# Optimization experiments

Hardware: AMD Instinct MI355X
Metric: run time of the kernel (lower is better)

The kernel has to match this reference:

```python
import jax, jax.numpy as jnp
import numpy as np
from jax import lax

N_DEV = 10

def _branch(inp, w, b, g, bt, m, v):
    # Conv2d(3->4,k3,s1,p1) + BatchNorm2d(eval stats) + ReLU + MaxPool2d(2)
    y = lax.conv_general_dilated(inp, w, (1, 1), ((1, 1), (1, 1)),
                                 dimension_numbers=('NCHW', 'OIHW', 'NCHW'))
    y = y + b[None, :, None, None]
    scale = (g / jnp.sqrt(v + 1e-5))[None, :, None, None]
    y = (y - m[None, :, None, None]) * scale + bt[None, :, None, None]
    y = jnp.maximum(y, 0.0)
    y = lax.reduce_window(y, -jnp.inf, lax.max, (1, 1, 2, 2), (1, 1, 2, 2), 'VALID')
    return y.reshape(y.shape[0], -1)

def _forward(x, conv_w, conv_b, bn_gamma, bn_beta, bn_mean, bn_var,
             cut_w_big, cut_w_small, fc1_w, fc1_b, fc2_w, fc2_b,
             out_w, out_b, b_mat, h_mat, a_mat, indicator, noise):
    zs = []
    for n in range(N_DEV):
        if n <= 1:
            inp = x[:, :, 32 * n:32 * n + 32, :32]
        else:
            r = (16 * (n - 2)) % 64
            c = 32 + 16 * ((n - 2) // 4)
            inp = x[:, :, r:r + 16, c:c + 16]
        flat = _branch(inp, conv_w[n], conv_b[n], bn_gamma[n], bn_beta[n],
                       bn_mean[n], bn_var[n])
        w = cut_w_big[n] if n <= 1 else cut_w_small[n - 2]
        zs.append(flat @ w.T)  # [B, 256]
    z = jnp.stack(zs)                           # [n_dev, B, 256]
    transmit = z * b_mat[:, None, :]            # per-device precoding
    # indicator is one-hot over subcarriers: h_sel[n, j] = h_mat[n, k(j)]
    h_sel = jnp.einsum('jk,nkc->njc', indicator, h_mat)   # [n_dev, 256, 5]
    # h_vec[n, j] = sum(a_mat[j].T @ h_sel[n, j])
    h_vec = jnp.einsum('njc,jcm->nj', h_sel, a_mat)       # [n_dev, 256]
    received = jnp.sum(transmit * h_vec[:, None, :], axis=0)  # [B, 256]
    noise_term = jnp.einsum('jc,jcm->j', noise, a_mat)        # [256]
    received = received + noise_term[None, :]
    h1 = jnp.maximum(received, 0.0)
    h2 = jnp.maximum(h1 @ fc1_w.T + fc1_b, 0.0)
    h3 = jnp.maximum(h2 @ fc2_w.T + fc2_b, 0.0)
    logits = h3 @ out_w.T + out_b
    return jax.nn.log_softmax(logits, axis=1)

def setup_inputs() -> dict:
    key = jax.random.key(0)
    ks = jax.random.split(key, 12)
    B, K, s = 4096, 64, 0.02
    return {
        'x': jax.random.normal(ks[0], (B, 3, 64, 64), jnp.float32),
        'conv_w': jax.random.normal(ks[1], (10, 4, 3, 3, 3), jnp.float32) * s,
        'conv_b': jnp.zeros((10, 4), jnp.float32),
        'bn_gamma': jnp.ones((10, 4), jnp.float32),
        'bn_beta': jnp.zeros((10, 4), jnp.float32),
        'bn_mean': jnp.zeros((10, 4), jnp.float32),
        'bn_var': jnp.ones((10, 4), jnp.float32),
        'cut_w_big': jax.random.normal(ks[2], (2, 256, 1024), jnp.float32) * s,
        'cut_w_small': jax.random.normal(ks[3], (8, 256, 256), jnp.float32) * s,
        'fc1_w': jax.random.normal(ks[4], (128, 256), jnp.float32) * s,
        'fc1_b': jnp.zeros((128,), jnp.float32),
        'fc2_w': jax.random.normal(ks[5], (64, 128), jnp.float32) * s,
        'fc2_b': jnp.zeros((64,), jnp.float32),
        'out_w': jax.random.normal(ks[6], (10, 64), jnp.float32) * s,
        'out_b': jnp.zeros((10,), jnp.float32),
        'b_mat': jax.random.normal(ks[7], (10, 256), jnp.float32) * 0.1,
        'h_mat': jax.random.normal(ks[8], (10, K, 5), jnp.float32),
        'a_mat': jax.random.normal(ks[9], (256, 5, 5), jnp.float32) * 0.1,
        'indicator': jax.nn.one_hot(
            jax.random.randint(ks[10], (256,), 0, K), K, dtype=jnp.float32),
        'noise': jax.random.normal(ks[11], (256, 5), jnp.float32) * 0.1,
    }

def reference(x, conv_w, conv_b, bn_gamma, bn_beta, bn_mean, bn_var,
              cut_w_big, cut_w_small, fc1_w, fc1_b, fc2_w, fc2_b,
              out_w, out_b, b_mat, h_mat, a_mat, indicator, noise):
    return _forward(x, conv_w, conv_b, bn_gamma, bn_beta, bn_mean, bn_var,
                    cut_w_big, cut_w_small, fc1_w, fc1_b, fc2_w, fc2_b,
                    out_w, out_b, b_mat, h_mat, a_mat, indicator, noise)
```

## Files before the change

### kernel.cpp

```cpp
#include <hip/hip_runtime.h>
#include <math.h>

typedef __attribute__((ext_vector_type(8))) short bf16x8;
typedef __attribute__((ext_vector_type(4))) float f32x4;

static __device__ __forceinline__ short f2bf(float f) {
    union { float f; unsigned u; } v; v.f = f;
    unsigned r = v.u + 0x7FFFu + ((v.u >> 16) & 1u);
    return (short)(r >> 16);
}

__global__ __launch_bounds__(256) void k_build_w(
    const float* __restrict__ cut_w_big,
    const float* __restrict__ cut_w_small,
    const float* __restrict__ b_mat,
    const float* __restrict__ h_mat,
    const float* __restrict__ a_mat,
    const float* __restrict__ indicator,
    short* __restrict__ W)
{
    int bx = blockIdx.x;
    int tid0 = bx << 8;
    int j = tid0 >> 12;
    int kbase = tid0 & 4095;
    int n = (kbase < 2048) ? (kbase >> 10) : 2 + ((kbase - 2048) >> 8);

    float arow[5];
#pragma unroll
    for (int c = 0; c < 5; ++c) {
        float s = 0.f;
#pragma unroll
        for (int m = 0; m < 5; ++m) s += a_mat[j * 25 + c * 5 + m];
        arow[c] = s;
    }
    int lane = threadIdx.x & 63;
    float hs = 0.f;
#pragma unroll
    for (int c = 0; c < 5; ++c) hs += h_mat[(n * 64 + lane) * 5 + c] * arow[c];
    float v = indicator[j * 64 + lane] * hs;
#pragma unroll
    for (int off = 32; off >= 1; off >>= 1) v += __shfl_xor(v, off);
    float coeff = b_mat[n * 256 + j] * v;

    int tid = tid0 + threadIdx.x;
    int k = tid & 4095;
    float w;
    if (k < 2048) {
        w = cut_w_big[(((k >> 10) * 256 + j) << 10) + (k & 1023)];
    } else {
        int kk = k - 2048;
        w = cut_w_small[(((kk >> 8) * 256 + j) << 8) + (kk & 255)];
    }
    W[tid] = f2bf(w * coeff);
}

__global__ __launch_bounds__(256) void k_branch(
    const float* __restrict__ x,
    const float* __restrict__ conv_w,
    const float* __restrict__ conv_b,
    const float* __restrict__ bn_g,
    const float* __restrict__ bn_b,
    const float* __restrict__ bn_m,
    const float* __restrict__ bn_v,
    short* __restrict__ F)
{
    __shared__ float in_s[4320];
    __shared__ float bn_a[4], bn_c[4];
    int t = threadIdx.x;
    int bx = blockIdx.x;

    for (int i = t; i < 4320; i += 256) in_s[i] = 0.f;
    __syncthreads();

    if (bx < 8192) {
        int n = bx >> 12;
        int b = bx & 4095;
        int r0 = 32 * n;
        for (int i = t; i < 3072; i += 256) {
            int ci = i >> 10;
            int rem = i & 1023;
            int yy = rem >> 5;
            int xx = rem & 31;
            in_s[ci * 1224 + (yy + 1) * 36 + (xx + 1)] =
                x[((size_t)(b * 3 + ci) * 64 + r0 + yy) * 64 + xx];
        }
        if (t < 4) {
            float scale = bn_g[n * 4 + t] * rsqrtf(bn_v[n * 4 + t] + 1e-5f);
            bn_a[t] = scale;
            bn_c[t] = (conv_b[n * 4 + t] - bn_m[n * 4 + t]) * scale + bn_b[n * 4 + t];
        }
        __syncthreads();

        int py = t >> 4, px = t & 15;
        float win[3][4][4];
#pragma unroll
        for (int ci = 0; ci < 3; ++ci)
#pragma unroll
            for (int dy = 0; dy < 4; ++dy)
#pragma unroll
                for (int dx = 0; dx < 4; ++dx)
                    win[ci][dy][dx] = in_s[ci * 1224 + (2 * py + dy) * 36 + (2 * px + dx)];
        const float* wp = conv_w + n * 108;
#pragma unroll
        for (int co = 0; co < 4; ++co) {
            float s00 = 0.f, s01 = 0.f, s10 = 0.f, s11 = 0.f;
#pragma unroll
            for (int ci = 0; ci < 3; ++ci)
#pragma unroll
                for (int ky = 0; ky < 3; ++ky)
#pragma unroll
                    for (int kx = 0; kx < 3; ++kx) {
                        float wv = wp[co * 27 + ci * 9 + ky * 3 + kx];
                        s00 += win[ci][ky][kx] * wv;
                        s01 += win[ci][ky][kx + 1] * wv;
                        s10 += win[ci][ky + 1][kx] * wv;
                        s11 += win[ci][ky + 1][kx + 1] * wv;
                    }
            float a = bn_a[co], c2 = bn_c[co];
            float v0 = fmaxf(s00 * a + c2, 0.f);
            float v1 = fmaxf(s01 * a + c2, 0.f);
            float v2 = fmaxf(s10 * a + c2, 0.f);
            float v3 = fmaxf(s11 * a + c2, 0.f);
            F[(size_t)b * 4096 + n * 1024 + co * 256 + t] =
                f2bf(fmaxf(fmaxf(v0, v1), fmaxf(v2, v3)));
        }
    } else {
        int i2 = bx - 8192;
        int n = 2 + (i2 >> 10);
        int g = i2 & 1023;
        int b0 = g * 4;
        int r0 = 16 * ((n - 2) & 3);
        int c0 = 32 + 16 * ((n - 2) >> 2);
        for (int i = t; i < 3072; i += 256) {
            int ci = i >> 10;
            int rem = i & 1023;
            int img = rem >> 8;
            int yy = (rem >> 4) & 15;
            int xx = rem & 15;
            in_s[((ci * 4 + img) * 18 + yy + 1) * 20 + xx + 1] =
                x[((size_t)((b0 + img) * 3 + ci) * 64 + r0 + yy) * 64 + c0 + xx];
        }
        if (t < 4) {
            float scale = bn_g[n * 4 + t] * rsqrtf(bn_v[n * 4 + t] + 1e-5f);
            bn_a[t] = scale;
            bn_c[t] = (conv_b[n * 4 + t] - bn_m[n * 4 + t]) * scale + bn_b[n * 4 + t];
        }
        __syncthreads();

        int img = t >> 6;
        int pos = t & 63;
        int py = pos >> 3, px = pos & 7;
        float win[3][4][4];
#pragma unroll
        for (int ci = 0; ci < 3; ++ci)
#pragma unroll
            for (int dy = 0; dy < 4; ++dy)
#pragma unroll
                for (int dx = 0; dx < 4; ++dx)
                    win[ci][dy][dx] =
                        in_s[((ci * 4 + img) * 18 + 2 * py + dy) * 20 + (2 * px + dx)];
        const float* wp = conv_w + n * 108;
#pragma unroll
        for (int co = 0; co < 4; ++co) {
            float s00 = 0.f, s01 = 0.f, s10 = 0.f, s11 = 0.f;
#pragma unroll
            for (int ci = 0; ci < 3; ++ci)
#pragma unroll
                for (int ky = 0; ky < 3; ++ky)
#pragma unroll
                    for (int kx = 0; kx < 3; ++kx) {
                        float wv = wp[co * 27 + ci * 9 + ky * 3 + kx];
                        s00 += win[ci][ky][kx] * wv;
                        s01 += win[ci][ky][kx + 1] * wv;
                        s10 += win[ci][ky + 1][kx] * wv;
                        s11 += win[ci][ky + 1][kx + 1] * wv;
                    }
            float a = bn_a[co], c2 = bn_c[co];
            float v0 = fmaxf(s00 * a + c2, 0.f);
            float v1 = fmaxf(s01 * a + c2, 0.f);
            float v2 = fmaxf(s10 * a + c2, 0.f);
            float v3 = fmaxf(s11 * a + c2, 0.f);
            F[(size_t)(b0 + img) * 4096 + 2048 + (n - 2) * 256 + co * 64 + pos] =
                f2bf(fmaxf(fmaxf(v0, v1), fmaxf(v2, v3)));
        }
    }
}

__global__ __launch_bounds__(256) void k_gemm(
    const short* __restrict__ F,
    const short* __restrict__ W,
    float* __restrict__ P)
{
    __shared__ short As[128 * 64];
    __shared__ short Bs[128 * 64];
    int bx = blockIdx.x;
    int mt = bx & 31;
    int jt = (bx >> 5) & 1;
    int ks = bx >> 6;
    int t = threadIdx.x;
    int m0 = mt << 7, j0 = jt << 7;

    int lane = t & 63;
    int wave = t >> 6;
    int wm = wave & 1, wn = wave >> 1;
    int l16 = lane & 15, quad = lane >> 4;

    f32x4 acc[4][4];
#pragma unroll
    for (int i = 0; i < 4; ++i)
#pragma unroll
        for (int j = 0; j < 4; ++j) acc[i][j] = (f32x4){0.f, 0.f, 0.f, 0.f};

    for (int it = 0; it < 8; ++it) {
        int k0 = (ks << 9) + (it << 6);
#pragma unroll
        for (int r = 0; r < 4; ++r) {
            int c = (r << 8) + t;
            int row = c >> 3, s = c & 7;
            int g = s ^ (row & 7);
            const short* gpA = F + ((size_t)(m0 + row) << 12) + k0 + (g << 3);
            const short* gpB = W + ((size_t)(j0 + row) << 12) + k0 + (g << 3);
            __builtin_amdgcn_global_load_lds(
                (const __attribute__((address_space(1))) void*)gpA,
                (__attribute__((address_space(3))) void*)(As + (c << 3)), 16, 0, 0);
            __builtin_amdgcn_global_load_lds(
                (const __attribute__((address_space(1))) void*)gpB,
                (__attribute__((address_space(3))) void*)(Bs + (c << 3)), 16, 0, 0);
        }
        __syncthreads();
#pragma unroll
        for (int ks2 = 0; ks2 < 2; ++ks2) {
            bf16x8 af[4], bfr[4];
#pragma unroll
            for (int mi = 0; mi < 4; ++mi) {
                int row = (wm << 6) + (mi << 4) + l16;
                int q = (ks2 << 2) + quad;
                int sl = q ^ (row & 7);
                af[mi] = *(const bf16x8*)&As[(row << 6) + (sl << 3)];
            }
#pragma unroll
            for (int ni = 0; ni < 4; ++ni) {
                int row = (wn << 6) + (ni << 4) + l16;
                int q = (ks2 << 2) + quad;
                int sl = q ^ (row & 7);
                bfr[ni] = *(const bf16x8*)&Bs[(row << 6) + (sl << 3)];
            }
#pragma unroll
            for (int mi = 0; mi < 4; ++mi)
#pragma unroll
                for (int ni = 0; ni < 4; ++ni)
                    acc[mi][ni] = __builtin_amdgcn_mfma_f32_16x16x32_bf16(
                        af[mi], bfr[ni], acc[mi][ni], 0, 0, 0);
        }
        __syncthreads();
    }

    float* Pp = P + ((size_t)ks << 20);
#pragma unroll
    for (int mi = 0; mi < 4; ++mi)
#pragma unroll
        for (int ni = 0; ni < 4; ++ni) {
            int col = j0 + (wn << 6) + (ni << 4) + l16;
#pragma unroll
            for (int r = 0; r < 4; ++r) {
                int row = m0 + (wm << 6) + (mi << 4) + (quad << 2) + r;
                Pp[(size_t)row * 256 + col] = acc[mi][ni][r];
            }
        }
}

__global__ __launch_bounds__(256) void k_reduce(
    const float* __restrict__ P,
    const float* __restrict__ a_mat,
    const float* __restrict__ noise,
    float* __restrict__ R)
{
    int b = blockIdx.x;
    int j = threadIdx.x;
    float nt = 0.f;
#pragma unroll
    for (int c = 0; c < 5; ++c) {
        float ar = 0.f;
#pragma unroll
        for (int m = 0; m < 5; ++m) ar += a_mat[j * 25 + c * 5 + m];
        nt += noise[j * 5 + c] * ar;
    }
    float s = nt;
    size_t base = (size_t)b * 256 + j;
#pragma unroll
    for (int ks = 0; ks < 8; ++ks) s += P[((size_t)ks << 20) + base];
    R[base] = fmaxf(s, 0.f);
}

__global__ __launch_bounds__(256) void k_mlp(
    const float* __restrict__ R,
    const float* __restrict__ fc1_w, const float* __restrict__ fc1_b,
    const float* __restrict__ fc2_w, const float* __restrict__ fc2_b,
    const float* __restrict__ out_w, const float* __restrict__ out_b,
    float* __restrict__ out)
{
    __shared__ __align__(16) float Rt[8][260];
    __shared__ __align__(16) float H2[8][132];
    __shared__ __align__(16) float H3[8][68];
    __shared__ float LG[8][12];
    __shared__ float mrow[8], srow[8];
    int t = threadIdx.x;
    int b0 = blockIdx.x * 8;

    for (int i = t; i < 512; i += 256) {
        int r = i >> 6;
        int c4 = i & 63;
        *(float4*)&Rt[r][c4 * 4] = *(const float4*)(R + (size_t)(b0 + r) * 256 + c4 * 4);
    }
    __syncthreads();

    for (int i = t; i < 1024; i += 256) {
        int r = i & 7, o = i >> 3;
        float s = fc1_b[o];
        const float* wpt = fc1_w + o * 256;
        for (int c = 0; c < 256; c += 4) {
            float4 wv = *(const float4*)(wpt + c);
            float4 rv = *(const float4*)&Rt[r][c];
            s += rv.x * wv.x + rv.y * wv.y + rv.z * wv.z + rv.w * wv.w;
        }
        H2[r][o] = fmaxf(s, 0.f);
    }
    __syncthreads();

    for (int i = t; i < 512; i += 256) {
        int r = i & 7, o = i >> 3;
        float s = fc2_b[o];
        const float* wpt = fc2_w + o * 128;
        for (int c = 0; c < 128; c += 4) {
            float4 wv = *(const float4*)(wpt + c);
            float4 rv = *(const float4*)&H2[r][c];
            s += rv.x * wv.x + rv.y * wv.y + rv.z * wv.z + rv.w * wv.w;
        }
        H3[r][o] = fmaxf(s, 0.f);
    }
    __syncthreads();

    if (t < 80) {
        int r = t & 7, o = t >> 3;
        float s = out_b[o];
        const float* wpt = out_w + o * 64;
        for (int c = 0; c < 64; c += 4) {
            float4 wv = *(const float4*)(wpt + c);
            float4 rv = *(const float4*)&H3[r][c];
            s += rv.x * wv.x + rv.y * wv.y + rv.z * wv.z + rv.w * wv.w;
        }
        LG[r][o] = s;
    }
    __syncthreads();

    if (t < 8) {
        float m = -1e30f;
#pragma unroll
        for (int o = 0; o < 10; ++o) m = fmaxf(m, LG[t][o]);
        float s = 0.f;
#pragma unroll
        for (int o = 0; o < 10; ++o) s += expf(LG[t][o] - m);
        mrow[t] = m;
        srow[t] = logf(s);
    }
    __syncthreads();

    if (t < 80) {
        int r = t & 7, o = t >> 3;
        out[(size_t)(b0 + r) * 10 + o] = LG[r][o] - mrow[r] - srow[r];
    }
}

extern "C" void kernel_launch(void* const* d_in, const int* in_sizes, int n_in,
                              void* d_out, int out_size, void* d_ws, size_t ws_size,
                              hipStream_t stream)
{
    const float* x           = (const float*)d_in[0];
    const float* conv_w      = (const float*)d_in[1];
    const float* conv_b      = (const float*)d_in[2];
    const float* bn_gamma    = (const float*)d_in[3];
    const float* bn_beta     = (const float*)d_in[4];
    const float* bn_mean     = (const float*)d_in[5];
    const float* bn_var      = (const float*)d_in[6];
    const float* cut_w_big   = (const float*)d_in[7];
    const float* cut_w_small = (const float*)d_in[8];
    const float* fc1_w       = (const float*)d_in[9];
    const float* fc1_b       = (const float*)d_in[10];
    const float* fc2_w       = (const float*)d_in[11];
    const float* fc2_b       = (const float*)d_in[12];
    const float* out_w       = (const float*)d_in[13];
    const float* out_b       = (const float*)d_in[14];
    const float* b_mat       = (const float*)d_in[15];
    const float* h_mat       = (const float*)d_in[16];
    const float* a_mat       = (const float*)d_in[17];
    const float* indicator   = (const float*)d_in[18];
    const float* noise       = (const float*)d_in[19];
    float* out = (float*)d_out;

    char* ws = (char*)d_ws;
    short* Fbf = (short*)ws;
    short* Wbf = (short*)(ws + 33554432);
    float* P   = (float*)(ws + 35651584);
    float* R   = (float*)(ws + 69206016);

    k_build_w<<<4096, 256, 0, stream>>>(cut_w_big, cut_w_small, b_mat, h_mat,
                                        a_mat, indicator, Wbf);
    k_branch<<<16384, 256, 0, stream>>>(x, conv_w, conv_b, bn_gamma, bn_beta,
                                        bn_mean, bn_var, Fbf);
    k_gemm<<<512, 256, 0, stream>>>(Fbf, Wbf, P);
    k_reduce<<<4096, 256, 0, stream>>>(P, a_mat, noise, R);
    k_mlp<<<512, 256, 0, stream>>>(R, fc1_w, fc1_b, fc2_w, fc2_b, out_w, out_b, out);
}
```

Before: 455.9 us.

## Fuse split-K reduce into MLP, vectorize conv loads/stores, permute feature layout

The split-K partial-sum reduction and noise term are folded into the MLP kernel, which removes one launch and the round trip of the R buffer through global memory. The conv branch kernel now zeroes only the halo borders instead of the whole tile, loads input with float4, and loops per input channel to cut register pressure. Its pooled outputs are written as packed short4 in a position-major, channel-minor layout. The weight-build kernel permutes its K index to match that new layout.

```diff
diff --git a/kernel.cpp b/kernel.cpp
--- a/kernel.cpp
+++ b/kernel.cpp
@@ -9,6 +9,7 @@
     unsigned r = v.u + 0x7FFFu + ((v.u >> 16) & 1u);
     return (short)(r >> 16);
 }
+
 
 __global__ __launch_bounds__(256) void k_build_w(
     const float* __restrict__ cut_w_big,
@@ -46,10 +47,16 @@
     int k = tid & 4095;
     float w;
     if (k < 2048) {
-        w = cut_w_big[(((k >> 10) * 256 + j) << 10) + (k & 1023)];
+        int nn = k >> 10;
+        int r = k & 1023;
+        int pos = r >> 2, co = r & 3;
+        w = cut_w_big[((nn * 256 + j) << 10) + co * 256 + pos];
     } else {
-        int kk = k - 2048;
-        w = cut_w_small[(((kk >> 8) * 256 + j) << 8) + (kk & 255)];
+        int kk2 = k - 2048;
+        int nn = kk2 >> 8;
+        int r = kk2 & 255;
+        int pos = r >> 2, co = r & 3;
+        w = cut_w_small[((nn * 256 + j) << 8) + co * 64 + pos];
     }
     W[tid] = f2bf(w * coeff);
 }
@@ -64,25 +71,29 @@
     const float* __restrict__ bn_v,
     short* __restrict__ F)
 {
-    __shared__ float in_s[4320];
+    __shared__ float in_s[5184];
     __shared__ float bn_a[4], bn_c[4];
     int t = threadIdx.x;
     int bx = blockIdx.x;
-
-    for (int i = t; i < 4320; i += 256) in_s[i] = 0.f;
-    __syncthreads();
 
     if (bx < 8192) {
         int n = bx >> 12;
         int b = bx & 4095;
         int r0 = 32 * n;
-        for (int i = t; i < 3072; i += 256) {
-            int ci = i >> 10;
-            int rem = i & 1023;
-            int yy = rem >> 5;
-            int xx = rem & 31;
-            in_s[ci * 1224 + (yy + 1) * 36 + (xx + 1)] =
-                x[((size_t)(b * 3 + ci) * 64 + r0 + yy) * 64 + xx];
+        for (int i = t; i < 408; i += 256) {
+            int ci = i / 136, rem = i % 136;
+            int seg = rem / 34, off = rem % 34;
+            int addr;
+            if (seg == 0)      addr = ci * 1360 + 3 + off;
+            else if (seg == 1) addr = ci * 1360 + 33 * 40 + 3 + off;
+            else if (seg == 2) addr = ci * 1360 + off * 40 + 3;
+            else               addr = ci * 1360 + off * 40 + 36;
+            in_s[addr] = 0.f;
+        }
+        for (int i = t; i < 768; i += 256) {
+            int ci = i >> 8, rem = i & 255, yy = rem >> 3, xq = rem & 7;
+            float4 v = *(const float4*)(x + ((size_t)(b * 3 + ci) * 64 + r0 + yy) * 64 + xq * 4);
+            *(float4*)&in_s[ci * 1360 + (yy + 1) * 40 + 4 + xq * 4] = v;
         }
         if (t < 4) {
             float scale = bn_g[n * 4 + t] * rsqrtf(bn_v[n * 4 + t] + 1e-5f);
@@ -92,38 +103,47 @@
         __syncthreads();
 
         int py = t >> 4, px = t & 15;
-        float win[3][4][4];
-#pragma unroll
-        for (int ci = 0; ci < 3; ++ci)
+        float s[4][4];
+#pragma unroll
+        for (int a = 0; a < 4; ++a)
+#pragma unroll
+            for (int p = 0; p < 4; ++p) s[a][p] = 0.f;
+        const float* wp = conv_w + n * 108;
+#pragma unroll
+        for (int ci = 0; ci < 3; ++ci) {
+            float wv[16];
+            int base = ci * 1360 + (2 * py) * 40 + 3 + 2 * px;
 #pragma unroll
             for (int dy = 0; dy < 4; ++dy)
 #pragma unroll
                 for (int dx = 0; dx < 4; ++dx)
-                    win[ci][dy][dx] = in_s[ci * 1224 + (2 * py + dy) * 36 + (2 * px + dx)];
-        const float* wp = conv_w + n * 108;
-#pragma unroll
-        for (int co = 0; co < 4; ++co) {
-            float s00 = 0.f, s01 = 0.f, s10 = 0.f, s11 = 0.f;
-#pragma unroll
-            for (int ci = 0; ci < 3; ++ci)
-#pragma unroll
-                for (int ky = 0; ky < 3; ++ky)
-#pragma unroll
-                    for (int kx = 0; kx < 3; ++kx) {
-                        float wv = wp[co * 27 + ci * 9 + ky * 3 + kx];
-                        s00 += win[ci][ky][kx] * wv;
-                        s01 += win[ci][ky][kx + 1] * wv;
-                        s10 += win[ci][ky + 1][kx] * wv;
-                        s11 += win[ci][ky + 1][kx + 1] * wv;
-                    }
-            float a = bn_a[co], c2 = bn_c[co];
-            float v0 = fmaxf(s00 * a + c2, 0.f);
-            float v1 = fmaxf(s01 * a + c2, 0.f);
-            float v2 = fmaxf(s10 * a + c2, 0.f);
-            float v3 = fmaxf(s11 * a + c2, 0.f);
-            F[(size_t)b * 4096 + n * 1024 + co * 256 + t] =
-                f2bf(fmaxf(fmaxf(v0, v1), fmaxf(v2, v3)));
-        }
+                    wv[dy * 4 + dx] = in_s[base + dy * 40 + dx];
+#pragma unroll
+            for (int co = 0; co < 4; ++co) {
+                const float* kk = wp + co * 27 + ci * 9;
+                float k0 = kk[0], k1 = kk[1], k2 = kk[2], k3 = kk[3], k4 = kk[4],
+                      k5 = kk[5], k6 = kk[6], k7 = kk[7], k8 = kk[8];
+                s[co][0] += wv[0] * k0 + wv[1] * k1 + wv[2] * k2 + wv[4] * k3 + wv[5] * k4 + wv[6] * k5 + wv[8] * k6 + wv[9] * k7 + wv[10] * k8;
+                s[co][1] += wv[1] * k0 + wv[2] * k1 + wv[3] * k2 + wv[5] * k3 + wv[6] * k4 + wv[7] * k5 + wv[9] * k6 + wv[10] * k7 + wv[11] * k8;
+                s[co][2] += wv[4] * k0 + wv[5] * k1 + wv[6] * k2 + wv[8] * k3 + wv[9] * k4 + wv[10] * k5 + wv[12] * k6 + wv[13] * k7 + wv[14] * k8;
+                s[co][3] += wv[5] * k0 + wv[6] * k1 + wv[7] * k2 + wv[9] * k3 + wv[10] * k4 + wv[11] * k5 + wv[13] * k6 + wv[14] * k7 + wv[15] * k8;
+            }
+        }
+        short4 pk;
+        {
+            float m[4];
+#pragma unroll
+            for (int co = 0; co < 4; ++co) {
+                float a = bn_a[co], c2 = bn_c[co];
+                float v0 = fmaxf(s[co][0] * a + c2, 0.f);
+                float v1 = fmaxf(s[co][1] * a + c2, 0.f);
+                float v2 = fmaxf(s[co][2] * a + c2, 0.f);
+                float v3 = fmaxf(s[co][3] * a + c2, 0.f);
+                m[co] = fmaxf(fmaxf(v0, v1), fmaxf(v2, v3));
+            }
+            pk.x = f2bf(m[0]); pk.y = f2bf(m[1]); pk.z = f2bf(m[2]); pk.w = f2bf(m[3]);
+        }
+        *(short4*)&F[(size_t)b * 4096 + n * 1024 + t * 4] = pk;
     } else {
         int i2 = bx - 8192;
         int n = 2 + (i2 >> 10);
@@ -131,14 +151,21 @@
         int b0 = g * 4;
         int r0 = 16 * ((n - 2) & 3);
         int c0 = 32 + 16 * ((n - 2) >> 2);
-        for (int i = t; i < 3072; i += 256) {
-            int ci = i >> 10;
-            int rem = i & 1023;
-            int img = rem >> 8;
-            int yy = (rem >> 4) & 15;
-            int xx = rem & 15;
-            in_s[((ci * 4 + img) * 18 + yy + 1) * 20 + xx + 1] =
-                x[((size_t)((b0 + img) * 3 + ci) * 64 + r0 + yy) * 64 + c0 + xx];
+        for (int i = t; i < 864; i += 256) {
+            int page = i / 72, rem = i % 72;
+            int seg = rem / 18, off = rem % 18;
+            int addr;
+            if (seg == 0)      addr = page * 432 + 3 + off;
+            else if (seg == 1) addr = page * 432 + 17 * 24 + 3 + off;
+            else if (seg == 2) addr = page * 432 + off * 24 + 3;
+            else               addr = page * 432 + off * 24 + 20;
+            in_s[addr] = 0.f;
+        }
+        for (int i = t; i < 768; i += 256) {
+            int page = i >> 6, rem = i & 63, yy = rem >> 2, xq = rem & 3;
+            int ci = page >> 2, img = page & 3;
+            float4 v = *(const float4*)(x + ((size_t)((b0 + img) * 3 + ci) * 64 + r0 + yy) * 64 + c0 + xq * 4);
+            *(float4*)&in_s[page * 432 + (yy + 1) * 24 + 4 + xq * 4] = v;
         }
         if (t < 4) {
             float scale = bn_g[n * 4 + t] * rsqrtf(bn_v[n * 4 + t] + 1e-5f);
@@ -150,39 +177,47 @@
         int img = t >> 6;
         int pos = t & 63;
         int py = pos >> 3, px = pos & 7;
-        float win[3][4][4];
-#pragma unroll
-        for (int ci = 0; ci < 3; ++ci)
+        float s[4][4];
+#pragma unroll
+        for (int a = 0; a < 4; ++a)
+#pragma unroll
+            for (int p = 0; p < 4; ++p) s[a][p] = 0.f;
+        const float* wp = conv_w + n * 108;
+#pragma unroll
+        for (int ci = 0; ci < 3; ++ci) {
+            float wv[16];
+            int base = (ci * 4 + img) * 432 + (2 * py) * 24 + 3 + 2 * px;
 #pragma unroll
             for (int dy = 0; dy < 4; ++dy)
 #pragma unroll
                 for (int dx = 0; dx < 4; ++dx)
-                    win[ci][dy][dx] =
-                        in_s[((ci * 4 + img) * 18 + 2 * py + dy) * 20 + (2 * px + dx)];
-        const float* wp = conv_w + n * 108;
-#pragma unroll
-        for (int co = 0; co < 4; ++co) {
-            float s00 = 0.f, s01 = 0.f, s10 = 0.f, s11 = 0.f;
-#pragma unroll
-            for (int ci = 0; ci < 3; ++ci)
-#pragma unroll
-                for (int ky = 0; ky < 3; ++ky)
-#pragma unroll
-                    for (int kx = 0; kx < 3; ++kx) {
-                        float wv = wp[co * 27 + ci * 9 + ky * 3 + kx];
-                        s00 += win[ci][ky][kx] * wv;
-                        s01 += win[ci][ky][kx + 1] * wv;
-                        s10 += win[ci][ky + 1][kx] * wv;
-                        s11 += win[ci][ky + 1][kx + 1] * wv;
-                    }
-            float a = bn_a[co], c2 = bn_c[co];
-            float v0 = fmaxf(s00 * a + c2, 0.f);
-            float v1 = fmaxf(s01 * a + c2, 0.f);
-            float v2 = fmaxf(s10 * a + c2, 0.f);
-            float v3 = fmaxf(s11 * a + c2, 0.f);
-            F[(size_t)(b0 + img) * 4096 + 2048 + (n - 2) * 256 + co * 64 + pos] =
-                f2bf(fmaxf(fmaxf(v0, v1), fmaxf(v2, v3)));
-        }
+                    wv[dy * 4 + dx] = in_s[base + dy * 24 + dx];
+#pragma unroll
+            for (int co = 0; co < 4; ++co) {
+                const float* kk = wp + co * 27 + ci * 9;
+                float k0 = kk[0], k1 = kk[1], k2 = kk[2], k3 = kk[3], k4 = kk[4],
+                      k5 = kk[5], k6 = kk[6], k7 = kk[7], k8 = kk[8];
+                s[co][0] += wv[0] * k0 + wv[1] * k1 + wv[2] * k2 + wv[4] * k3 + wv[5] * k4 + wv[6] * k5 + wv[8] * k6 + wv[9] * k7 + wv[10] * k8;
+                s[co][1] += wv[1] * k0 + wv[2] * k1 + wv[3] * k2 + wv[5] * k3 + wv[6] * k4 + wv[7] * k5 + wv[9] * k6 + wv[10] * k7 + wv[11] * k8;
+                s[co][2] += wv[4] * k0 + wv[5] * k1 + wv[6] * k2 + wv[8] * k3 + wv[9] * k4 + wv[10] * k5 + wv[12] * k6 + wv[13] * k7 + wv[14] * k8;
+                s[co][3] += wv[5] * k0 + wv[6] * k1 + wv[7] * k2 + wv[9] * k3 + wv[10] * k4 + wv[11] * k5 + wv[13] * k6 + wv[14] * k7 + wv[15] * k8;
+            }
+        }
+        short4 pk;
+        {
+            float m[4];
+#pragma unroll
+            for (int co = 0; co < 4; ++co) {
+                float a = bn_a[co], c2 = bn_c[co];
+                float v0 = fmaxf(s[co][0] * a + c2, 0.f);
+                float v1 = fmaxf(s[co][1] * a + c2, 0.f);
+                float v2 = fmaxf(s[co][2] * a + c2, 0.f);
+                float v3 = fmaxf(s[co][3] * a + c2, 0.f);
+                m[co] = fmaxf(fmaxf(v0, v1), fmaxf(v2, v3));
+            }
+            pk.x = f2bf(m[0]); pk.y = f2bf(m[1]); pk.z = f2bf(m[2]); pk.w = f2bf(m[3]);
+        }
+        *(short4*)&F[(size_t)(b0 + img) * 4096 + 2048 + (n - 2) * 256 + pos * 4] = pk;
     }
 }
 
@@ -216,10 +251,10 @@
 #pragma unroll
         for (int r = 0; r < 4; ++r) {
             int c = (r << 8) + t;
-            int row = c >> 3, s = c & 7;
-            int g = s ^ (row & 7);
-            const short* gpA = F + ((size_t)(m0 + row) << 12) + k0 + (g << 3);
-            const short* gpB = W + ((size_t)(j0 + row) << 12) + k0 + (g << 3);
+            int row = c >> 3, sgl = c & 7;
+            int gsw = sgl ^ (row & 7);
+            const short* gpA = F + ((size_t)(m0 + row) << 12) + k0 + (gsw << 3);
+            const short* gpB = W + ((size_t)(j0 + row) << 12) + k0 + (gsw << 3);
             __builtin_amdgcn_global_load_lds(
                 (const __attribute__((address_space(1))) void*)gpA,
                 (__attribute__((address_space(3))) void*)(As + (c << 3)), 16, 0, 0);
@@ -269,31 +304,10 @@
         }
 }
 
-__global__ __launch_bounds__(256) void k_reduce(
+__global__ __launch_bounds__(256) void k_mlp(
     const float* __restrict__ P,
     const float* __restrict__ a_mat,
     const float* __restrict__ noise,
-    float* __restrict__ R)
-{
-    int b = blockIdx.x;
-    int j = threadIdx.x;
-    float nt = 0.f;
-#pragma unroll
-    for (int c = 0; c < 5; ++c) {
-        float ar = 0.f;
-#pragma unroll
-        for (int m = 0; m < 5; ++m) ar += a_mat[j * 25 + c * 5 + m];
-        nt += noise[j * 5 + c] * ar;
-    }
-    float s = nt;
-    size_t base = (size_t)b * 256 + j;
-#pragma unroll
-    for (int ks = 0; ks < 8; ++ks) s += P[((size_t)ks << 20) + base];
-    R[base] = fmaxf(s, 0.f);
-}
-
-__global__ __launch_bounds__(256) void k_mlp(
-    const float* __restrict__ R,
     const float* __restrict__ fc1_w, const float* __restrict__ fc1_b,
     const float* __restrict__ fc2_w, const float* __restrict__ fc2_b,
     const float* __restrict__ out_w, const float* __restrict__ out_b,
@@ -304,13 +318,36 @@
     __shared__ __align__(16) float H3[8][68];
     __shared__ float LG[8][12];
     __shared__ float mrow[8], srow[8];
+    __shared__ float nts[256];
     int t = threadIdx.x;
     int b0 = blockIdx.x * 8;
+
+    {
+        float nt = 0.f;
+#pragma unroll
+        for (int c = 0; c < 5; ++c) {
+            float ar = 0.f;
+#pragma unroll
+            for (int m = 0; m < 5; ++m) ar += a_mat[t * 25 + c * 5 + m];
+            nt += noise[t * 5 + c] * ar;
+        }
+        nts[t] = nt;
+    }
+    __syncthreads();
 
     for (int i = t; i < 512; i += 256) {
         int r = i >> 6;
         int c4 = i & 63;
-        *(float4*)&Rt[r][c4 * 4] = *(const float4*)(R + (size_t)(b0 + r) * 256 + c4 * 4);
+        size_t base = (size_t)(b0 + r) * 256 + c4 * 4;
+        float4 sum = *(const float4*)&nts[c4 * 4];
+#pragma unroll
+        for (int ks = 0; ks < 8; ++ks) {
+            float4 p = *(const float4*)(P + ((size_t)ks << 20) + base);
+            sum.x += p.x; sum.y += p.y; sum.z += p.z; sum.w += p.w;
+        }
+        sum.x = fmaxf(sum.x, 0.f); sum.y = fmaxf(sum.y, 0.f);
+        sum.z = fmaxf(sum.z, 0.f); sum.w = fmaxf(sum.w, 0.f);
+        *(float4*)&Rt[r][c4 * 4] = sum;
     }
     __syncthreads();
 
@@ -401,13 +438,12 @@
     short* Fbf = (short*)ws;
     short* Wbf = (short*)(ws + 33554432);
     float* P   = (float*)(ws + 35651584);
-    float* R   = (float*)(ws + 69206016);
 
     k_build_w<<<4096, 256, 0, stream>>>(cut_w_big, cut_w_small, b_mat, h_mat,
                                         a_mat, indicator, Wbf);
     k_branch<<<16384, 256, 0, stream>>>(x, conv_w, conv_b, bn_gamma, bn_beta,
                                         bn_mean, bn_var, Fbf);
     k_gemm<<<512, 256, 0, stream>>>(Fbf, Wbf, P);
-    k_reduce<<<4096, 256, 0, stream>>>(P, a_mat, noise, R);
-    k_mlp<<<512, 256, 0, stream>>>(R, fc1_w, fc1_b, fc2_w, fc2_b, out_w, out_b, out);
-}
+    k_mlp<<<512, 256, 0, stream>>>(P, a_mat, noise, fc1_w, fc1_b, fc2_w, fc2_b,
+                                   out_w, out_b, out);
+}
```

Measured after the change: 423.2 us. 7.2% less time.
